# Kernel tuning notes

Hardware: AMD Instinct MI355X
Metric: run time of the kernel (lower is better)

Reference implementation:

```python
import jax, jax.numpy as jnp
import numpy as np

N, T, D_ENC, D_DEC, U = 32, 2048, 1024, 1024, 1024


def setup_inputs() -> dict:
    key = jax.random.key(0)
    k1, k2, k3, k4, k5, k6 = jax.random.split(key, 6)
    queries = jax.random.normal(k1, (N, 1, D_DEC), dtype=jnp.float32)
    encoder_output = jax.random.normal(k2, (N, T, D_ENC), dtype=jnp.float32)
    # lengths in [1, T] so every row has at least one valid position
    lengths = jax.random.randint(k3, (N,), 1, T + 1, dtype=jnp.int32)
    v = jax.random.normal(k4, (U,), dtype=jnp.float32)
    # torch Linear weights are [out, in]; y = x @ W.T
    Wq = jax.random.normal(k5, (U, D_DEC), dtype=jnp.float32) * (1.0 / np.sqrt(D_DEC))
    Wk = jax.random.normal(k6, (U, D_ENC), dtype=jnp.float32) * (1.0 / np.sqrt(D_ENC))
    return {"queries": queries, "encoder_output": encoder_output,
            "lengths": lengths, "v": v, "Wq": Wq, "Wk": Wk}


def reference(queries, encoder_output, lengths, v, Wq, Wk):
    # set_memory: project keys, build padding mask
    proj_key = jnp.einsum('nte,ue->ntu', encoder_output, Wk)      # [N,T,U]
    mask = jnp.arange(T)[None, :] >= lengths[:, None]             # [N,T] True = masked

    # forward (normalize=False path)
    proj_query = jnp.einsum('nqd,ud->nqu', queries, Wq)           # [N,1,U]
    weights = jnp.tanh(proj_query + proj_key) @ v                 # [N,T]
    weights = jnp.where(mask, -jnp.inf, weights)
    alignments = jax.nn.softmax(weights, axis=-1)                 # [N,T]
    contexts = jnp.einsum('nt,nte->ne', alignments, encoder_output)  # [N,D_enc]
    return contexts, alignments
```

## Files before the change

kernel.cpp:

```cpp
#include <hip/hip_runtime.h>
#include <hip/hip_bf16.h>

#define NB 32
#define TD 2048
#define DIM 1024

typedef _Float16 v8h __attribute__((ext_vector_type(8)));
typedef _Float16 v4h __attribute__((ext_vector_type(4)));
typedef float    v4f __attribute__((ext_vector_type(4)));

__device__ __forceinline__ float ftanh(float x) {
    x = fminf(15.f, fmaxf(-15.f, x));
    float e = __expf(2.f * x);
    return (e - 1.f) / (e + 1.f);
}

__device__ __forceinline__ void gld_lds16(const void* g, void* l) {
    __builtin_amdgcn_global_load_lds(
        (const __attribute__((address_space(1))) unsigned int*)g,
        (__attribute__((address_space(3))) unsigned int*)l, 16, 0, 0);
}

__global__ __launch_bounds__(256) void pq_kernel(const float* __restrict__ q,
                                                 const float* __restrict__ Wq,
                                                 float* __restrict__ pq) {
    int wid  = blockIdx.x * 4 + (threadIdx.x >> 6);
    int lane = threadIdx.x & 63;
    int n = wid >> 10;
    int u = wid & 1023;
    const float4* qr = (const float4*)(q  + (size_t)n * DIM);
    const float4* wr = (const float4*)(Wq + (size_t)u * DIM);
    float s = 0.f;
#pragma unroll
    for (int j = 0; j < 4; ++j) {
        int i = lane + 64 * j;
        float4 a = qr[i], b = wr[i];
        s += a.x * b.x + a.y * b.y + a.z * b.z + a.w * b.w;
    }
#pragma unroll
    for (int off = 32; off >= 1; off >>= 1) s += __shfl_xor(s, off);
    if (lane == 0) pq[(size_t)n * DIM + u] = s;
}

__global__ __launch_bounds__(256) void cvt_kernel(const float* __restrict__ enc,
                                                  const float* __restrict__ Wk,
                                                  const int* __restrict__ lengths,
                                                  _Float16* __restrict__ ench,
                                                  _Float16* __restrict__ wkh) {
    int flat = threadIdx.x * 32;
    int rsub = flat >> 10;
    int col  = flat & 1023;
    const float* src;
    _Float16* dst;
    size_t row;
    if (blockIdx.x < 8192) {
        row = (size_t)blockIdx.x * 8 + rsub;
        int n = (int)(row >> 11), t = (int)(row & 2047);
        if (t >= lengths[n]) return;
        src = enc; dst = ench;
    } else {
        row = (size_t)(blockIdx.x - 8192) * 8 + rsub;
        src = Wk; dst = wkh;
    }
    const float4* s = (const float4*)(src + row * DIM + col);
    _Float16* d = dst + row * DIM + col;
#pragma unroll
    for (int g = 0; g < 4; ++g) {
        float4 a = s[2 * g], b = s[2 * g + 1];
        v8h h;
        h[0] = (_Float16)a.x; h[1] = (_Float16)a.y; h[2] = (_Float16)a.z; h[3] = (_Float16)a.w;
        h[4] = (_Float16)b.x; h[5] = (_Float16)b.y; h[6] = (_Float16)b.z; h[7] = (_Float16)b.w;
        *(v8h*)(d + g * 8) = h;
    }
}

__global__ __launch_bounds__(512) void gemm_tanh_h3(
        const _Float16* __restrict__ ench, const _Float16* __restrict__ wkh,
        const float* __restrict__ pq, const float* __restrict__ v,
        const int* __restrict__ lengths, float* __restrict__ weights) {
    const int bm = blockIdx.x;
    const int bn = blockIdx.y;
    const int rowBase = bm * 256;
    const int n = rowBase >> 11;
    const int tstart = rowBase & 2047;
    if (lengths[n] <= tstart) return;

    __shared__ _Float16 As[256 * 32];
    __shared__ _Float16 Bs[128 * 32];

    const int tid  = threadIdx.x;
    const int lane = tid & 63;
    const int wv   = tid >> 6;
    const int wm   = wv >> 1, wn = wv & 1;
    const int q4   = lane >> 4;
    const int l16  = lane & 15;

    v4f acc[4][4];
    const v4f vz = {0.f, 0.f, 0.f, 0.f};
#pragma unroll
    for (int i = 0; i < 4; ++i)
#pragma unroll
        for (int j = 0; j < 4; ++j) acc[i][j] = vz;

    const int srow = (lane >> 2);
    const int skc  = (lane & 3) * 8;
    const _Float16* Ag = ench + (size_t)rowBase * DIM;
    const _Float16* Bg = wkh + (size_t)bn * 128 * DIM;

    for (int k0 = 0; k0 < DIM; k0 += 32) {
        __syncthreads();
#pragma unroll
        for (int j = 0; j < 2; ++j) {
            int row = wv * 32 + j * 16 + srow;
            gld_lds16(Ag + (size_t)row * DIM + k0 + skc, &As[wv * 1024 + j * 512]);
        }
        {
            int row = wv * 16 + srow;
            gld_lds16(Bg + (size_t)row * DIM + k0 + skc, &Bs[wv * 512]);
        }
        __syncthreads();

        v8h afr[4], bfr[4];
#pragma unroll
        for (int mt = 0; mt < 4; ++mt)
            afr[mt] = *(const v8h*)(&As[(wm * 64 + mt * 16 + l16) * 32 + q4 * 8]);
#pragma unroll
        for (int nt = 0; nt < 4; ++nt)
            bfr[nt] = *(const v8h*)(&Bs[(wn * 64 + nt * 16 + l16) * 32 + q4 * 8]);
#pragma unroll
        for (int mt = 0; mt < 4; ++mt)
#pragma unroll
            for (int nt = 0; nt < 4; ++nt)
                acc[mt][nt] = __builtin_amdgcn_mfma_f32_16x16x32_f16(
                    afr[mt], bfr[nt], acc[mt][nt], 0, 0, 0);
    }

    float pqv[4], vv[4];
#pragma unroll
    for (int nt = 0; nt < 4; ++nt) {
        int ug = bn * 128 + wn * 64 + nt * 16 + l16;
        pqv[nt] = pq[(size_t)n * DIM + ug];
        vv[nt]  = v[ug];
    }
#pragma unroll
    for (int mt = 0; mt < 4; ++mt) {
#pragma unroll
        for (int r = 0; r < 4; ++r) {
            float s = 0.f;
#pragma unroll
            for (int nt = 0; nt < 4; ++nt)
                s += ftanh(acc[mt][nt][r] + pqv[nt]) * vv[nt];
            s += __shfl_xor(s, 1);
            s += __shfl_xor(s, 2);
            s += __shfl_xor(s, 4);
            s += __shfl_xor(s, 8);
            if (l16 == 0) {
                int R = rowBase + wm * 64 + mt * 16 + q4 * 4 + r;
                atomicAdd(&weights[R], s);
            }
        }
    }
}

__global__ __launch_bounds__(256) void gemm_tanh_kernel(
        const float* __restrict__ enc, const float* __restrict__ Wk,
        const float* __restrict__ pq,  const float* __restrict__ v,
        const int* __restrict__ lengths, float* __restrict__ weights) {
    const int bm = blockIdx.x;
    const int bn = blockIdx.y;
    const int rowBase = bm * 128;
    const int n = rowBase >> 11;
    const int tstart = rowBase & 2047;
    if (lengths[n] <= tstart) return;

    __shared__ _Float16 As[128 * 40];
    __shared__ _Float16 Bs[128 * 40];

    const int tid  = threadIdx.x;
    const int lane = tid & 63;
    const int wv   = tid >> 6;
    const int wm   = wv >> 1, wn = wv & 1;
    const int q4   = lane >> 4;
    const int l16  = lane & 15;

    v4f acc[4][4];
    const v4f vz = {0.f, 0.f, 0.f, 0.f};
#pragma unroll
    for (int i = 0; i < 4; ++i)
#pragma unroll
        for (int j = 0; j < 4; ++j) acc[i][j] = vz;

    const int srow = tid >> 3;
    const int skc  = (tid & 7) * 4;

    for (int k0 = 0; k0 < DIM; k0 += 32) {
        __syncthreads();
#pragma unroll
        for (int j = 0; j < 4; ++j) {
            int row = j * 32 + srow;
            float4 av = *(const float4*)(enc + (size_t)(rowBase + row) * DIM + k0 + skc);
            v4h ah;
            ah.x = (_Float16)av.x; ah.y = (_Float16)av.y;
            ah.z = (_Float16)av.z; ah.w = (_Float16)av.w;
            *(v4h*)(&As[row * 40 + skc]) = ah;
            float4 bv = *(const float4*)(Wk + (size_t)(bn * 128 + row) * DIM + k0 + skc);
            v4h bh;
            bh.x = (_Float16)bv.x; bh.y = (_Float16)bv.y;
            bh.z = (_Float16)bv.z; bh.w = (_Float16)bv.w;
            *(v4h*)(&Bs[row * 40 + skc]) = bh;
        }
        __syncthreads();

        v8h afr[4], bfr[4];
#pragma unroll
        for (int mt = 0; mt < 4; ++mt)
            afr[mt] = *(const v8h*)(&As[(wm * 64 + mt * 16 + l16) * 40 + q4 * 8]);
#pragma unroll
        for (int nt = 0; nt < 4; ++nt)
            bfr[nt] = *(const v8h*)(&Bs[(wn * 64 + nt * 16 + l16) * 40 + q4 * 8]);
#pragma unroll
        for (int mt = 0; mt < 4; ++mt)
#pragma unroll
            for (int nt = 0; nt < 4; ++nt)
                acc[mt][nt] = __builtin_amdgcn_mfma_f32_16x16x32_f16(
                    afr[mt], bfr[nt], acc[mt][nt], 0, 0, 0);
    }

    float pqv[4], vv[4];
#pragma unroll
    for (int nt = 0; nt < 4; ++nt) {
        int ug = bn * 128 + wn * 64 + nt * 16 + l16;
        pqv[nt] = pq[(size_t)n * DIM + ug];
        vv[nt]  = v[ug];
    }
#pragma unroll
    for (int mt = 0; mt < 4; ++mt) {
#pragma unroll
        for (int r = 0; r < 4; ++r) {
            float s = 0.f;
#pragma unroll
            for (int nt = 0; nt < 4; ++nt)
                s += ftanh(acc[mt][nt][r] + pqv[nt]) * vv[nt];
            s += __shfl_xor(s, 1);
            s += __shfl_xor(s, 2);
            s += __shfl_xor(s, 4);
            s += __shfl_xor(s, 8);
            if (l16 == 0) {
                int R = rowBase + wm * 64 + mt * 16 + q4 * 4 + r;
                atomicAdd(&weights[R], s);
            }
        }
    }
}

__global__ __launch_bounds__(256) void softmax_kernel(float* __restrict__ w,
                                                      const int* __restrict__ lengths) {
    int n = blockIdx.x;
    int len = lengths[n];
    float* row = w + (size_t)n * TD;
    int tid = threadIdx.x;
    float wv[8], ev[8];
    float mx = -INFINITY;
#pragma unroll
    for (int i = 0; i < 8; ++i) {
        int t = tid + i * 256;
        float x = row[t];
        x = (t < len) ? x : -INFINITY;
        wv[i] = x;
        mx = fmaxf(mx, x);
    }
#pragma unroll
    for (int off = 32; off >= 1; off >>= 1) mx = fmaxf(mx, __shfl_xor(mx, off));
    __shared__ float redm[4], reds[4];
    int lane = tid & 63, wvid = tid >> 6;
    if (lane == 0) redm[wvid] = mx;
    __syncthreads();
    mx = fmaxf(fmaxf(redm[0], redm[1]), fmaxf(redm[2], redm[3]));
    float sm = 0.f;
#pragma unroll
    for (int i = 0; i < 8; ++i) { ev[i] = __expf(wv[i] - mx); sm += ev[i]; }
#pragma unroll
    for (int off = 32; off >= 1; off >>= 1) sm += __shfl_xor(sm, off);
    if (lane == 0) reds[wvid] = sm;
    __syncthreads();
    sm = reds[0] + reds[1] + reds[2] + reds[3];
    float inv = 1.f / sm;
#pragma unroll
    for (int i = 0; i < 8; ++i) row[tid + i * 256] = ev[i] * inv;
}

__global__ __launch_bounds__(256) void ctx_kernel_h(const float* __restrict__ align,
                                                    const _Float16* __restrict__ ench,
                                                    const int* __restrict__ lengths,
                                                    float* __restrict__ ctx) {
    int n  = blockIdx.y;
    int t0 = blockIdx.x * 32;
    int len = lengths[n];
    if (len <= t0) return;
    int e = threadIdx.x * 4;
    float4 acc = make_float4(0.f, 0.f, 0.f, 0.f);
    const float* arow = align + (size_t)n * TD;
    const _Float16* erow = ench + (size_t)n * TD * DIM;
    int tend = min(t0 + 32, len);
    for (int t = t0; t < tend; ++t) {
        float a = arow[t];
        v4h ev = *(const v4h*)(erow + (size_t)t * DIM + e);
        acc.x += a * (float)ev[0]; acc.y += a * (float)ev[1];
        acc.z += a * (float)ev[2]; acc.w += a * (float)ev[3];
    }
    float* c = ctx + (size_t)n * DIM + e;
    atomicAdd(c + 0, acc.x);
    atomicAdd(c + 1, acc.y);
    atomicAdd(c + 2, acc.z);
    atomicAdd(c + 3, acc.w);
}

__global__ __launch_bounds__(256) void ctx_kernel(const float* __restrict__ align,
                                                  const float* __restrict__ enc,
                                                  const int* __restrict__ lengths,
                                                  float* __restrict__ ctx) {
    int n  = blockIdx.y;
    int t0 = blockIdx.x * 128;
    if (lengths[n] <= t0) return;
    int e = threadIdx.x * 4;
    float4 acc = make_float4(0.f, 0.f, 0.f, 0.f);
    const float* arow = align + (size_t)n * TD;
    const float* erow = enc + (size_t)n * TD * DIM;
    for (int tt = 0; tt < 128; ++tt) {
        int t = t0 + tt;
        float a = arow[t];
        if (a != 0.f) {
            float4 evv = *(const float4*)(erow + (size_t)t * DIM + e);
            acc.x += a * evv.x; acc.y += a * evv.y;
            acc.z += a * evv.z; acc.w += a * evv.w;
        }
    }
    float* c = ctx + (size_t)n * DIM + e;
    atomicAdd(c + 0, acc.x);
    atomicAdd(c + 1, acc.y);
    atomicAdd(c + 2, acc.z);
    atomicAdd(c + 3, acc.w);
}

extern "C" void kernel_launch(void* const* d_in, const int* in_sizes, int n_in,
                              void* d_out, int out_size, void* d_ws, size_t ws_size,
                              hipStream_t stream) {
    const float* queries = (const float*)d_in[0];
    const float* enc     = (const float*)d_in[1];
    const int*   lengths = (const int*)d_in[2];
    const float* v       = (const float*)d_in[3];
    const float* Wq      = (const float*)d_in[4];
    const float* Wk      = (const float*)d_in[5];

    float* out = (float*)d_out;
    float* ctx = out;
    float* alg = out + NB * DIM;
    (void)in_sizes; (void)n_in; (void)out_size;

    const size_t ench_elems = (size_t)NB * TD * DIM;
    const size_t wkh_elems  = (size_t)DIM * DIM;
    const size_t need = (ench_elems + wkh_elems) * sizeof(_Float16)
                      + (size_t)NB * DIM * sizeof(float);

    hipMemsetAsync(alg, 0, (size_t)NB * TD * sizeof(float), stream);

    if (ws_size >= need) {
        _Float16* ench = (_Float16*)d_ws;
        _Float16* wkh  = ench + ench_elems;
        float*    pq   = (float*)(wkh + wkh_elems);
        hipMemsetAsync(ctx, 0, (size_t)NB * DIM * sizeof(float), stream);
        pq_kernel<<<NB * DIM / 4, 256, 0, stream>>>(queries, Wq, pq);
        cvt_kernel<<<8192 + 128, 256, 0, stream>>>(enc, Wk, lengths, ench, wkh);
        dim3 g2(256, 8);
        gemm_tanh_h3<<<g2, 512, 0, stream>>>(ench, wkh, pq, v, lengths, alg);
        softmax_kernel<<<NB, 256, 0, stream>>>(alg, lengths);
        ctx_kernel_h<<<dim3(64, NB), 256, 0, stream>>>(alg, ench, lengths, ctx);
    } else {
        float* pq = ctx;
        pq_kernel<<<NB * DIM / 4, 256, 0, stream>>>(queries, Wq, pq);
        dim3 g2(512, 8);
        gemm_tanh_kernel<<<g2, 256, 0, stream>>>(enc, Wk, pq, v, lengths, alg);
        softmax_kernel<<<NB, 256, 0, stream>>>(alg, lengths);
        hipMemsetAsync(ctx, 0, (size_t)NB * DIM * sizeof(float), stream);
        ctx_kernel<<<dim3(16, NB), 256, 0, stream>>>(alg, enc, lengths, ctx);
    }
}
```

Baseline: 582.7 us.

## Replace LDS-staged GEMM with single-wave direct-global-load MFMA tiles

The fp16 key-projection GEMM no longer stages tiles through shared memory with block-wide barriers. Each 64-thread workgroup now computes a 64x128 tile and loads MFMA fragments straight from global memory into registers. The grid becomes 8 column blocks by 1024 row blocks, with blockIdx.x over columns so the row blocks that share A data run close together and can hit in L2. This removes the LDS traffic and __syncthreads cost, but it gives up cross-wave data reuse, relies on cache for operand reuse, and the 32 accumulators raise register pressure.

Measured after the change: 632.3 us. 1.09x slower.

```diff
diff --git a/kernel.cpp b/kernel.cpp
--- a/kernel.cpp
+++ b/kernel.cpp
@@ -13,12 +13,6 @@
     x = fminf(15.f, fmaxf(-15.f, x));
     float e = __expf(2.f * x);
     return (e - 1.f) / (e + 1.f);
-}
-
-__device__ __forceinline__ void gld_lds16(const void* g, void* l) {
-    __builtin_amdgcn_global_load_lds(
-        (const __attribute__((address_space(1))) unsigned int*)g,
-        (__attribute__((address_space(3))) unsigned int*)l, 16, 0, 0);
 }
 
 __global__ __launch_bounds__(256) void pq_kernel(const float* __restrict__ q,
@@ -74,71 +68,51 @@
     }
 }
 
-__global__ __launch_bounds__(512) void gemm_tanh_h3(
+__global__ __launch_bounds__(64, 2) void gemm_tanh_w(
         const _Float16* __restrict__ ench, const _Float16* __restrict__ wkh,
         const float* __restrict__ pq, const float* __restrict__ v,
         const int* __restrict__ lengths, float* __restrict__ weights) {
-    const int bm = blockIdx.x;
-    const int bn = blockIdx.y;
-    const int rowBase = bm * 256;
+    const int bn = blockIdx.x;
+    const int bm = blockIdx.y;
+    const int rowBase = bm * 64;
     const int n = rowBase >> 11;
-    const int tstart = rowBase & 2047;
-    if (lengths[n] <= tstart) return;
-
-    __shared__ _Float16 As[256 * 32];
-    __shared__ _Float16 Bs[128 * 32];
-
-    const int tid  = threadIdx.x;
-    const int lane = tid & 63;
-    const int wv   = tid >> 6;
-    const int wm   = wv >> 1, wn = wv & 1;
+    if (lengths[n] <= (rowBase & 2047)) return;
+
+    const int lane = threadIdx.x;
     const int q4   = lane >> 4;
     const int l16  = lane & 15;
 
-    v4f acc[4][4];
+    v4f acc[4][8];
     const v4f vz = {0.f, 0.f, 0.f, 0.f};
 #pragma unroll
     for (int i = 0; i < 4; ++i)
 #pragma unroll
-        for (int j = 0; j < 4; ++j) acc[i][j] = vz;
-
-    const int srow = (lane >> 2);
-    const int skc  = (lane & 3) * 8;
-    const _Float16* Ag = ench + (size_t)rowBase * DIM;
-    const _Float16* Bg = wkh + (size_t)bn * 128 * DIM;
-
+        for (int j = 0; j < 8; ++j) acc[i][j] = vz;
+
+    const _Float16* Ab = ench + (((size_t)(rowBase + l16)) << 10) + q4 * 8;
+    const _Float16* Bb = wkh + (((size_t)(bn * 128 + l16)) << 10) + q4 * 8;
+
+#pragma unroll 2
     for (int k0 = 0; k0 < DIM; k0 += 32) {
-        __syncthreads();
-#pragma unroll
-        for (int j = 0; j < 2; ++j) {
-            int row = wv * 32 + j * 16 + srow;
-            gld_lds16(Ag + (size_t)row * DIM + k0 + skc, &As[wv * 1024 + j * 512]);
-        }
-        {
-            int row = wv * 16 + srow;
-            gld_lds16(Bg + (size_t)row * DIM + k0 + skc, &Bs[wv * 512]);
-        }
-        __syncthreads();
-
-        v8h afr[4], bfr[4];
+        v8h af[4], bf[8];
 #pragma unroll
         for (int mt = 0; mt < 4; ++mt)
-            afr[mt] = *(const v8h*)(&As[(wm * 64 + mt * 16 + l16) * 32 + q4 * 8]);
-#pragma unroll
-        for (int nt = 0; nt < 4; ++nt)
-            bfr[nt] = *(const v8h*)(&Bs[(wn * 64 + nt * 16 + l16) * 32 + q4 * 8]);
+            af[mt] = *(const v8h*)(Ab + ((size_t)(mt * 16) << 10) + k0);
+#pragma unroll
+        for (int nt = 0; nt < 8; ++nt)
+            bf[nt] = *(const v8h*)(Bb + ((size_t)(nt * 16) << 10) + k0);
 #pragma unroll
         for (int mt = 0; mt < 4; ++mt)
 #pragma unroll
-            for (int nt = 0; nt < 4; ++nt)
+            for (int nt = 0; nt < 8; ++nt)
                 acc[mt][nt] = __builtin_amdgcn_mfma_f32_16x16x32_f16(
-                    afr[mt], bfr[nt], acc[mt][nt], 0, 0, 0);
-    }
-
-    float pqv[4], vv[4];
-#pragma unroll
-    for (int nt = 0; nt < 4; ++nt) {
-        int ug = bn * 128 + wn * 64 + nt * 16 + l16;
+                    af[mt], bf[nt], acc[mt][nt], 0, 0, 0);
+    }
+
+    float pqv[8], vv[8];
+#pragma unroll
+    for (int nt = 0; nt < 8; ++nt) {
+        int ug = bn * 128 + nt * 16 + l16;
         pqv[nt] = pq[(size_t)n * DIM + ug];
         vv[nt]  = v[ug];
     }
@@ -148,14 +122,14 @@
         for (int r = 0; r < 4; ++r) {
             float s = 0.f;
 #pragma unroll
-            for (int nt = 0; nt < 4; ++nt)
+            for (int nt = 0; nt < 8; ++nt)
                 s += ftanh(acc[mt][nt][r] + pqv[nt]) * vv[nt];
             s += __shfl_xor(s, 1);
             s += __shfl_xor(s, 2);
             s += __shfl_xor(s, 4);
             s += __shfl_xor(s, 8);
             if (l16 == 0) {
-                int R = rowBase + wm * 64 + mt * 16 + q4 * 4 + r;
+                int R = rowBase + mt * 16 + q4 * 4 + r;
                 atomicAdd(&weights[R], s);
             }
         }
@@ -371,8 +345,8 @@
         hipMemsetAsync(ctx, 0, (size_t)NB * DIM * sizeof(float), stream);
         pq_kernel<<<NB * DIM / 4, 256, 0, stream>>>(queries, Wq, pq);
         cvt_kernel<<<8192 + 128, 256, 0, stream>>>(enc, Wk, lengths, ench, wkh);
-        dim3 g2(256, 8);
-        gemm_tanh_h3<<<g2, 512, 0, stream>>>(ench, wkh, pq, v, lengths, alg);
+        dim3 g2(8, 1024);
+        gemm_tanh_w<<<g2, 64, 0, stream>>>(ench, wkh, pq, v, lengths, alg);
         softmax_kernel<<<NB, 256, 0, stream>>>(alg, lengths);
         ctx_kernel_h<<<dim3(64, NB), 256, 0, stream>>>(alg, ench, lengths, ctx);
     } else {
```
